# Kernel tuning notes

Measured on AMD Instinct MI355X. Metric: run time of the kernel, lower is better.

## Reference

```python
import jax, jax.numpy as jnp
import numpy as np

B, N, D_MODEL, H, LIN_K = 4, 4096, 1024, 16, 256
D_K = D_MODEL // H


def setup_inputs() -> dict:
    key = jax.random.key(0)
    ks = jax.random.split(key, 9)
    s = 1.0 / np.sqrt(D_MODEL)
    return {
        "K": jax.random.normal(ks[0], (B, N, D_MODEL), jnp.float32),
        "Q": jax.random.normal(ks[1], (B, N, D_MODEL), jnp.float32),
        "V": jax.random.normal(ks[2], (B, N, D_MODEL), jnp.float32),
        "We": jax.random.normal(ks[3], (N, LIN_K), jnp.float32) / np.sqrt(N),
        "be": jnp.zeros((LIN_K,), jnp.float32),
        "Wf": jax.random.normal(ks[4], (N, LIN_K), jnp.float32) / np.sqrt(N),
        "bf": jnp.zeros((LIN_K,), jnp.float32),
        "Wo": jax.random.normal(ks[5], (D_MODEL, D_MODEL), jnp.float32) * s,
        "bo": jnp.zeros((D_MODEL,), jnp.float32),
        "n_heads": H,
    }


def reference(K, Q, V, We, be, Wf, bf, Wo, bo, n_heads):
    b, n, d_model = K.shape
    d_k = d_model // n_heads
    split = lambda x: x.reshape(b, n, n_heads, d_k).transpose(0, 2, 1, 3)  # [b,h,n,d]
    Kh, Qh, Vh = split(K), split(Q), split(V)
    # Linformer projection: Dense(k) applied to K^T [b,h,d,n] -> [b,h,d,k]
    Kp = jnp.einsum("bhnd,nk->bhdk", Kh, We) + be
    scores = jnp.einsum("bhnd,bhdk->bhnk", Qh, Kp) / jnp.sqrt(jnp.float32(d_k))
    P = jax.nn.softmax(scores, axis=-1)  # dropout rate 0.0 -> identity
    # V projection: Dense(k) on V^T then transpose back -> [b,h,k,d]
    Vp = jnp.einsum("bhnd,nk->bhkd", Vh, Wf) + bf[:, None]
    out = jnp.einsum("bhnk,bhkd->bhnd", P, Vp)
    out = out.transpose(0, 2, 1, 3).reshape(b, n, d_model)
    return out @ Wo + bo
```

## Files before the change

### kernel.cpp

```cpp
#include <hip/hip_runtime.h>
#include <hip/hip_bf16.h>

#define BB      4
#define SEQ     4096
#define DMODEL  1024
#define NHEAD   16
#define DK      64
#define LK      256
#define BH      (BB*NHEAD)
#define SPLITK  4

typedef unsigned short u16;
typedef unsigned int   u32;
typedef float f32x4  __attribute__((ext_vector_type(4)));
typedef _Float16 f16x8 __attribute__((ext_vector_type(8)));

__device__ __forceinline__ u16 f2h(float f) {
    _Float16 h = (_Float16)f;
    u16 r; __builtin_memcpy(&r, &h, 2); return r;
}
__device__ __forceinline__ u32 packh(float a, float b) {
    return (u32)f2h(a) | ((u32)f2h(b) << 16);
}
__device__ __forceinline__ f16x8 pack8h(float4 a, float4 b) {
    union { uint4 u; f16x8 h; } r;
    r.u = make_uint4(packh(a.x, a.y), packh(a.z, a.w),
                     packh(b.x, b.y), packh(b.z, b.w));
    return r.h;
}
__device__ __forceinline__ void gl2lds16(const void* g, void* l) {
    __builtin_amdgcn_global_load_lds(
        (const __attribute__((address_space(1))) unsigned int*)g,
        (__attribute__((address_space(3))) unsigned int*)l,
        16, 0, 0);
}

__device__ __forceinline__ void tconv_body(
    const float* __restrict__ S, u16* __restrict__ D,
    int ss, int ds, int r0, int c0, int t)
{
    __shared__ float T[64][65];
    {
        int rr = (t >> 4) * 4;
        int cc = (t & 15) * 4;
#pragma unroll
        for (int i = 0; i < 4; ++i) {
            float4 v = *(const float4*)(S + (size_t)(r0 + rr + i) * ss + c0 + cc);
            T[rr + i][cc + 0] = v.x; T[rr + i][cc + 1] = v.y;
            T[rr + i][cc + 2] = v.z; T[rr + i][cc + 3] = v.w;
        }
    }
    __syncthreads();
    int cr = t >> 2, rc = (t & 3) * 16;
    u32 o[8];
#pragma unroll
    for (int j = 0; j < 8; ++j)
        o[j] = packh(T[rc + 2 * j][cr], T[rc + 2 * j + 1][cr]);
    u16* d = D + (size_t)(c0 + cr) * ds + r0 + rc;
    *(uint4*)(d)     = make_uint4(o[0], o[1], o[2], o[3]);
    *(uint4*)(d + 8) = make_uint4(o[4], o[5], o[6], o[7]);
}

__global__ __launch_bounds__(256) void tconv(
    const float* __restrict__ src, u16* __restrict__ dst,
    int ss, int ds, size_t sbo, size_t dbo)
{
    tconv_body(src + (size_t)blockIdx.z * sbo, dst + (size_t)blockIdx.z * dbo,
               ss, ds, blockIdx.x * 64, blockIdx.y * 64, threadIdx.x);
}

__global__ __launch_bounds__(256) void wo_convert(
    const float* __restrict__ Wo, u16* __restrict__ WoT)
{
    tconv_body(Wo, WoT, DMODEL, DMODEL, blockIdx.y * 64, blockIdx.x * 64, threadIdx.x);
}

__global__ __launch_bounds__(256) void tconv_all(
    const float* __restrict__ We, const float* __restrict__ Wf,
    const float* __restrict__ K,  const float* __restrict__ V,
    const float* __restrict__ Wo,
    u16* __restrict__ WeT, u16* __restrict__ WfT,
    u16* __restrict__ KT,  u16* __restrict__ VT, u16* __restrict__ WoT)
{
    const int id = blockIdx.x;
    const float* S; u16* D; int ss, ds, r0, c0;
    if (id < 512) {
        int j = id & 255;
        S  = (id < 256) ? We : Wf;
        D  = (id < 256) ? WeT : WfT;
        ss = LK; ds = SEQ;
        r0 = (j & 63) * 64; c0 = (j >> 6) * 64;
    } else if (id < 8704) {
        int j  = id - 512;
        int isV = j >= 4096; if (isV) j -= 4096;
        int bz = j >> 10, rem = j & 1023;
        S  = (isV ? V : K) + (size_t)bz * SEQ * DMODEL;
        D  = (isV ? VT : KT) + (size_t)bz * DMODEL * SEQ;
        ss = DMODEL; ds = SEQ;
        r0 = (rem & 63) * 64; c0 = (rem >> 6) * 64;
    } else {
        int j = id - 8704;
        S = Wo; D = WoT; ss = DMODEL; ds = DMODEL;
        r0 = (j & 15) * 64; c0 = (j >> 4) * 64;
    }
    tconv_body(S, D, ss, ds, r0, c0, threadIdx.x);
}

#define PROJ_BODY(Ab, Bb, bias, Cb, bias_on_row, c_row_stride, c0, r0)          \
    const int t  = threadIdx.x;                                                 \
    const int lane = t & 63;                                                    \
    const int w  = t >> 6;                                                      \
    const int wr = w >> 1, wc = w & 1;                                          \
    const int q  = lane >> 4, c = lane & 15;                                    \
    __shared__ u16 As[2][128 * 64];                                             \
    __shared__ u16 Bs[2][128 * 64];                                             \
    auto stage = [&](int buf, int kk) {                                         \
        _Pragma("unroll")                                                       \
        for (int i = 0; i < 4; ++i) {                                           \
            int li  = i * 256 + t;                                              \
            int row = li >> 3;                                                  \
            int c8  = (li & 7) ^ (row & 7);                                     \
            gl2lds16(Ab + (size_t)(r0 + row) * SEQ + kk + c8 * 8, &As[buf][(size_t)li * 8]); \
            gl2lds16(Bb + (size_t)(c0 + row) * SEQ + kk + c8 * 8, &Bs[buf][(size_t)li * 8]); \
        }                                                                       \
    };                                                                          \
    f32x4 acc[4][4];                                                            \
    _Pragma("unroll")                                                           \
    for (int m = 0; m < 4; ++m)                                                 \
        _Pragma("unroll")                                                       \
        for (int n = 0; n < 4; ++n) acc[m][n] = (f32x4){0.f, 0.f, 0.f, 0.f};    \
    stage(0, 0);                                                                \
    __syncthreads();                                                            \
    int cur = 0;                                                                \
    for (int k0 = 0; k0 < SEQ; k0 += 64) {                                      \
        if (k0 + 64 < SEQ) stage(cur ^ 1, k0 + 64);                             \
        _Pragma("unroll")                                                       \
        for (int s = 0; s < 2; ++s) {                                           \
            f16x8 af[4], bf[4];                                                 \
            _Pragma("unroll")                                                   \
            for (int m = 0; m < 4; ++m) {                                       \
                int row = wr * 64 + m * 16 + c;                                 \
                int c8  = (s * 4 + q) ^ (row & 7);                              \
                af[m] = *(const f16x8*)&As[cur][row * 64 + c8 * 8];             \
            }                                                                   \
            _Pragma("unroll")                                                   \
            for (int n = 0; n < 4; ++n) {                                       \
                int row = wc * 64 + n * 16 + c;                                 \
                int c8  = (s * 4 + q) ^ (row & 7);                              \
                bf[n] = *(const f16x8*)&Bs[cur][row * 64 + c8 * 8];             \
            }                                                                   \
            _Pragma("unroll")                                                   \
            for (int m = 0; m < 4; ++m)                                         \
                _Pragma("unroll")                                               \
                for (int n = 0; n < 4; ++n)                                     \
                    acc[m][n] = __builtin_amdgcn_mfma_f32_16x16x32_f16(af[m], bf[n], acc[m][n], 0, 0, 0); \
        }                                                                       \
        __syncthreads();                                                        \
        cur ^= 1;                                                               \
    }                                                                           \
    if (bias_on_row) {                                                          \
        _Pragma("unroll")                                                       \
        for (int m = 0; m < 4; ++m) {                                           \
            int rowb = r0 + wr * 64 + m * 16 + q * 4;                           \
            _Pragma("unroll")                                                   \
            for (int r = 0; r < 4; ++r) {                                       \
                float bv = bias[rowb + r];                                      \
                u16* dst = Cb + (size_t)(rowb + r) * c_row_stride + c0 + wc * 64 + c; \
                _Pragma("unroll")                                               \
                for (int n = 0; n < 4; ++n) dst[n * 16] = f2h(acc[m][n][r] + bv); \
            }                                                                   \
        }                                                                       \
    } else {                                                                    \
        float bv[4];                                                            \
        _Pragma("unroll")                                                       \
        for (int n = 0; n < 4; ++n) bv[n] = bias[c0 + wc * 64 + n * 16 + c];    \
        _Pragma("unroll")                                                       \
        for (int m = 0; m < 4; ++m) {                                           \
            int rowb = r0 + wr * 64 + m * 16 + q * 4;                           \
            _Pragma("unroll")                                                   \
            for (int r = 0; r < 4; ++r) {                                       \
                u16* dst = Cb + (size_t)(rowb + r) * c_row_stride + c0 + wc * 64 + c; \
                _Pragma("unroll")                                               \
                for (int n = 0; n < 4; ++n) dst[n * 16] = f2h(acc[m][n][r] + bv[n]); \
            }                                                                   \
        }                                                                       \
    }

__global__ __launch_bounds__(256) void proj_gemm(
    const u16* __restrict__ A, const u16* __restrict__ B,
    const float* __restrict__ bias, u16* __restrict__ Cout,
    int bias_on_row, size_t a_batch, size_t b_batch,
    int c_row_stride, size_t c_batch)
{
    const u16* Ab = A + (size_t)blockIdx.z * a_batch;
    const u16* Bb = B + (size_t)blockIdx.z * b_batch;
    u16* Cb       = Cout + (size_t)blockIdx.z * c_batch;
    const int c0 = blockIdx.x * 128;
    const int r0 = blockIdx.y * 128;
    PROJ_BODY(Ab, Bb, bias, Cb, bias_on_row, c_row_stride, c0, r0)
}

__global__ __launch_bounds__(256) void proj_both(
    const u16* __restrict__ WeT, const u16* __restrict__ WfT,
    const u16* __restrict__ KT,  const u16* __restrict__ VT,
    const float* __restrict__ be, const float* __restrict__ bfp,
    u16* __restrict__ KpF, u16* __restrict__ VpF)
{
    const int id = blockIdx.x;
    const u16 *Ab, *Bb; const float* bias; u16* Cb;
    int bias_on_row, c_row_stride, c0, r0;
    if (id < 64) {
        int b = id >> 4, s = id & 15;
        c0 = (s & 7) * 128; r0 = (s >> 3) * 128;
        Ab = WeT; Bb = KT + (size_t)b * DMODEL * SEQ;
        bias = be; bias_on_row = 1;
        Cb = KpF + (size_t)b * LK * DMODEL; c_row_stride = DMODEL;
    } else {
        int j = id - 64, b = j >> 4, s = j & 15;
        c0 = (s & 1) * 128; r0 = (s >> 1) * 128;
        Ab = VT + (size_t)b * DMODEL * SEQ; Bb = WfT;
        bias = bfp; bias_on_row = 0;
        Cb = VpF + (size_t)b * DMODEL * LK; c_row_stride = LK;
    }
    PROJ_BODY(Ab, Bb, bias, Cb, bias_on_row, c_row_stride, c0, r0)
}

__global__ __launch_bounds__(256) void proj_split(
    const u16* __restrict__ WeT, const u16* __restrict__ WfT,
    const u16* __restrict__ KT,  const u16* __restrict__ VT,
    float* __restrict__ PPK, float* __restrict__ PPV)
{
    const int sk = blockIdx.x >> 7;
    const int id = blockIdx.x & 127;
    const u16 *Ab, *Bb; float* Pout;
    int crs, c0, r0;
    if (id < 64) {
        int b = id >> 4, s = id & 15;
        c0 = (s & 7) * 128; r0 = (s >> 3) * 128;
        Ab = WeT; Bb = KT + (size_t)b * DMODEL * SEQ;
        Pout = PPK + ((size_t)sk * BB + b) * (LK * DMODEL); crs = DMODEL;
    } else {
        int j = id - 64, b = j >> 4, s = j & 15;
        c0 = (s & 1) * 128; r0 = (s >> 1) * 128;
        Ab = VT + (size_t)b * DMODEL * SEQ; Bb = WfT;
        Pout = PPV + ((size_t)sk * BB + b) * (DMODEL * LK); crs = LK;
    }
    const int kbeg = sk * (SEQ / SPLITK), kend = kbeg + SEQ / SPLITK;

    const int t  = threadIdx.x;
    const int lane = t & 63;
    const int w  = t >> 6;
    const int wr = w >> 1, wc = w & 1;
    const int q  = lane >> 4, c = lane & 15;
    __shared__ u16 As[2][128 * 64];
    __shared__ u16 Bs[2][128 * 64];
    auto stage = [&](int buf, int kk) {
#pragma unroll
        for (int i = 0; i < 4; ++i) {
            int li  = i * 256 + t;
            int row = li >> 3;
            int c8  = (li & 7) ^ (row & 7);
            gl2lds16(Ab + (size_t)(r0 + row) * SEQ + kk + c8 * 8, &As[buf][(size_t)li * 8]);
            gl2lds16(Bb + (size_t)(c0 + row) * SEQ + kk + c8 * 8, &Bs[buf][(size_t)li * 8]);
        }
    };
    f32x4 acc[4][4];
#pragma unroll
    for (int m = 0; m < 4; ++m)
#pragma unroll
        for (int n = 0; n < 4; ++n) acc[m][n] = (f32x4){0.f, 0.f, 0.f, 0.f};
    stage(0, kbeg);
    __syncthreads();
    int cur = 0;
    for (int k0 = kbeg; k0 < kend; k0 += 64) {
        if (k0 + 64 < kend) stage(cur ^ 1, k0 + 64);
#pragma unroll
        for (int s = 0; s < 2; ++s) {
            f16x8 af[4], bf[4];
#pragma unroll
            for (int m = 0; m < 4; ++m) {
                int row = wr * 64 + m * 16 + c;
                int c8  = (s * 4 + q) ^ (row & 7);
                af[m] = *(const f16x8*)&As[cur][row * 64 + c8 * 8];
            }
#pragma unroll
            for (int n = 0; n < 4; ++n) {
                int row = wc * 64 + n * 16 + c;
                int c8  = (s * 4 + q) ^ (row & 7);
                bf[n] = *(const f16x8*)&Bs[cur][row * 64 + c8 * 8];
            }
#pragma unroll
            for (int m = 0; m < 4; ++m)
#pragma unroll
                for (int n = 0; n < 4; ++n)
                    acc[m][n] = __builtin_amdgcn_mfma_f32_16x16x32_f16(af[m], bf[n], acc[m][n], 0, 0, 0);
        }
        __syncthreads();
        cur ^= 1;
    }
#pragma unroll
    for (int m = 0; m < 4; ++m) {
        int rowb = r0 + wr * 64 + m * 16 + q * 4;
#pragma unroll
        for (int r = 0; r < 4; ++r) {
            float* dst = Pout + (size_t)(rowb + r) * crs + c0 + wc * 64 + c;
#pragma unroll
            for (int n = 0; n < 4; ++n) dst[n * 16] = acc[m][n][r];
        }
    }
}

__global__ __launch_bounds__(256) void proj_reduce(
    const float* __restrict__ PPK, const float* __restrict__ PPV,
    const float* __restrict__ be,  const float* __restrict__ bfp,
    u16* __restrict__ KpF, u16* __restrict__ VpF)
{
    const int isV = blockIdx.y;
    const float* P    = isV ? PPV : PPK;
    const float* bias = isV ? bfp : be;
    u16* Out          = isV ? VpF : KpF;
    const size_t flat = ((size_t)blockIdx.x * 256 + threadIdx.x) * 4;
    const size_t skstride = (size_t)BB * LK * DMODEL;
    float4 a = *(const float4*)(P + flat);
#pragma unroll
    for (int sk = 1; sk < SPLITK; ++sk) {
        float4 p = *(const float4*)(P + (size_t)sk * skstride + flat);
        a.x += p.x; a.y += p.y; a.z += p.z; a.w += p.w;
    }
    if (!isV) {
        float bv = bias[(flat >> 10) & 255];
        a.x += bv; a.y += bv; a.z += bv; a.w += bv;
    } else {
        float4 bv = *(const float4*)(bias + (flat & 255));
        a.x += bv.x; a.y += bv.y; a.z += bv.z; a.w += bv.w;
    }
    uint2 o = make_uint2(packh(a.x, a.y), packh(a.z, a.w));
    *(uint2*)(Out + flat) = o;
}

__global__ __launch_bounds__(512) void attn_mfma(
    const float* __restrict__ Qin, const u16* __restrict__ KpF,
    const u16* __restrict__ VpF,   u16* __restrict__ AO)
{
    const int lin = blockIdx.x + blockIdx.y * gridDim.x;
    const int tid = (lin & 7) * 32 + (lin >> 3);
    const int bh = tid >> 2, b = bh >> 4, h = bh & 15;
    const int n0 = (tid & 3) * 1024;
    const int t  = threadIdx.x;
    const int w    = t >> 6;
    const int lane = t & 63;
    const int q    = lane >> 4;
    const int c    = lane & 15;

    __shared__ u16 Kl[16384];
    __shared__ u16 Vl[16384];
    __shared__ u16 Pl[128 * 264];

    const u16* kbase = KpF + (size_t)b * LK * DMODEL + h * DK;
#pragma unroll
    for (int i = 0; i < 4; ++i) {
        int li = i * 512 + t;
        int row = li >> 3, ch = li & 7;
        int chs = ch ^ (row & 7);
        gl2lds16(kbase + (size_t)row * DMODEL + chs * 8, Kl + (size_t)li * 8);
    }
    const u16* vbase = VpF + ((size_t)b * DMODEL + h * DK) * LK;
#pragma unroll
    for (int i = 0; i < 4; ++i) {
        int li = i * 512 + t;
        int row = li >> 5, ch = li & 31;
        int chs = (ch & 24) | ((ch & 7) ^ (row & 7));
        gl2lds16(vbase + (size_t)row * LK + chs * 8, Vl + (size_t)li * 8);
    }
    __syncthreads();

    const float* qbase = Qin + ((size_t)b * SEQ + n0 + w * 16 + c) * DMODEL + h * DK;
    const float4* qp0 = (const float4*)qbase;
    float4 q0 = qp0[2 * q], q1 = qp0[2 * q + 1];
    float4 q2 = qp0[8 + 2 * q], q3 = qp0[8 + 2 * q + 1];

    for (int p = 0; p < 8; ++p) {
        f16x8 a0 = pack8h(q0, q1);
        f16x8 a1 = pack8h(q2, q3);
        if (p < 7) {
            const float4* qp = (const float4*)(qbase + (size_t)(p + 1) * 128 * DMODEL);
            q0 = qp[2 * q]; q1 = qp[2 * q + 1];
            q2 = qp[8 + 2 * q]; q3 = qp[8 + 2 * q + 1];
        }

        f32x4 sc[16];
#pragma unroll
        for (int nt = 0; nt < 16; ++nt) sc[nt] = (f32x4){0.f, 0.f, 0.f, 0.f};
#pragma unroll
        for (int nt = 0; nt < 16; ++nt) {
            int ra = (nt * 16 + c) * 64;
            f16x8 b0 = *(const f16x8*)&Kl[ra + ((q ^ (c & 7)) * 8)];
            f16x8 b1 = *(const f16x8*)&Kl[ra + (((4 + q) ^ (c & 7)) * 8)];
            sc[nt] = __builtin_amdgcn_mfma_f32_16x16x32_f16(a0, b0, sc[nt], 0, 0, 0);
            sc[nt] = __builtin_amdgcn_mfma_f32_16x16x32_f16(a1, b1, sc[nt], 0, 0, 0);
        }

        float mx[4] = {-1e30f, -1e30f, -1e30f, -1e30f};
#pragma unroll
        for (int nt = 0; nt < 16; ++nt) {
            sc[nt] *= 0.125f;
#pragma unroll
            for (int r = 0; r < 4; ++r) mx[r] = fmaxf(mx[r], sc[nt][r]);
        }
#pragma unroll
        for (int d = 1; d < 16; d <<= 1)
#pragma unroll
            for (int r = 0; r < 4; ++r) mx[r] = fmaxf(mx[r], __shfl_xor(mx[r], d, 64));

        float sm[4] = {0.f, 0.f, 0.f, 0.f};
#pragma unroll
        for (int nt = 0; nt < 16; ++nt)
#pragma unroll
            for (int r = 0; r < 4; ++r) {
                float e = __expf(sc[nt][r] - mx[r]);
                sc[nt][r] = e;
                sm[r] += e;
            }
#pragma unroll
        for (int d = 1; d < 16; d <<= 1)
#pragma unroll
            for (int r = 0; r < 4; ++r) sm[r] += __shfl_xor(sm[r], d, 64);
        float inv[4];
#pragma unroll
        for (int r = 0; r < 4; ++r) inv[r] = 1.0f / sm[r];

#pragma unroll
        for (int nt = 0; nt < 16; ++nt)
#pragma unroll
            for (int r = 0; r < 4; ++r)
                Pl[(w * 16 + q * 4 + r) * 264 + nt * 16 + c] = f2h(sc[nt][r] * inv[r]);

        f32x4 ov[4];
#pragma unroll
        for (int nt = 0; nt < 4; ++nt) ov[nt] = (f32x4){0.f, 0.f, 0.f, 0.f};
#pragma unroll
        for (int ks = 0; ks < 8; ++ks) {
            f16x8 pa = *(const f16x8*)&Pl[(w * 16 + c) * 264 + ks * 32 + q * 8];
#pragma unroll
            for (int nt = 0; nt < 4; ++nt) {
                int chunk = ks * 4 + q;
                int chs = (chunk & 24) | ((chunk & 7) ^ (c & 7));
                f16x8 vf = *(const f16x8*)&Vl[(nt * 16 + c) * 256 + chs * 8];
                ov[nt] = __builtin_amdgcn_mfma_f32_16x16x32_f16(pa, vf, ov[nt], 0, 0, 0);
            }
        }

#pragma unroll
        for (int nt = 0; nt < 4; ++nt)
#pragma unroll
            for (int r = 0; r < 4; ++r)
                Pl[(w * 16 + q * 4 + r) * 264 + nt * 16 + c] = f2h(ov[nt][r]);

#pragma unroll
        for (int ps = 0; ps < 2; ++ps) {
            int lr  = w * 16 + ps * 8 + (lane >> 3);
            int col = (lane & 7) * 8;
            uint4 vv = *(uint4*)&Pl[lr * 264 + col];
            *(uint4*)(AO + ((size_t)b * SEQ + n0 + p * 128 + lr) * DMODEL + h * DK + col) = vv;
        }
    }
}

#define OBM 128
#define OBN 128
#define OBK 64

__global__ __launch_bounds__(256) void out_gemm_mfma(
    const u16* __restrict__ AO, const u16* __restrict__ WoT,
    const float* __restrict__ bo, float* __restrict__ Out)
{
    const int lin = blockIdx.x + blockIdx.y * gridDim.x;
    const int tid = (lin & 7) * 128 + (lin >> 3);
    const int r0 = (tid >> 3) * OBM;
    const int c0 = (tid & 7) * OBN;
    const int t  = threadIdx.x;
    const int lane = t & 63;
    const int w  = t >> 6;
    const int wr = w >> 1, wc = w & 1;
    const int q  = lane >> 4, c = lane & 15;

    __shared__ u16 As[OBM * OBK];
    __shared__ u16 Bs[OBN * OBK];

    f32x4 acc[4][4];
#pragma unroll
    for (int m = 0; m < 4; ++m)
#pragma unroll
        for (int n = 0; n < 4; ++n) acc[m][n] = (f32x4){0.f, 0.f, 0.f, 0.f};

    for (int k0 = 0; k0 < DMODEL; k0 += OBK) {
#pragma unroll
        for (int i = 0; i < 4; ++i) {
            int li  = i * 256 + t;
            int row = li >> 3;
            int c8  = (li & 7) ^ (row & 7);
            gl2lds16(AO  + (size_t)(r0 + row) * DMODEL + k0 + c8 * 8, (u16*)As + (size_t)li * 8);
            gl2lds16(WoT + (size_t)(c0 + row) * DMODEL + k0 + c8 * 8, (u16*)Bs + (size_t)li * 8);
        }
        __syncthreads();

#pragma unroll
        for (int s = 0; s < 2; ++s) {
            f16x8 af[4], bf[4];
#pragma unroll
            for (int m = 0; m < 4; ++m) {
                int row = wr * 64 + m * 16 + c;
                int c8  = (s * 4 + q) ^ (row & 7);
                af[m] = *(const f16x8*)&As[row * 64 + c8 * 8];
            }
#pragma unroll
            for (int n = 0; n < 4; ++n) {
                int row = wc * 64 + n * 16 + c;
                int c8  = (s * 4 + q) ^ (row & 7);
                bf[n] = *(const f16x8*)&Bs[row * 64 + c8 * 8];
            }
#pragma unroll
            for (int m = 0; m < 4; ++m)
#pragma unroll
                for (int n = 0; n < 4; ++n)
                    acc[m][n] = __builtin_amdgcn_mfma_f32_16x16x32_f16(af[m], bf[n], acc[m][n], 0, 0, 0);
        }
        __syncthreads();
    }

    float bv[4];
#pragma unroll
    for (int n = 0; n < 4; ++n) bv[n] = bo[c0 + wc * 64 + n * 16 + c];
#pragma unroll
    for (int m = 0; m < 4; ++m) {
        int rowb = r0 + wr * 64 + m * 16 + q * 4;
#pragma unroll
        for (int r = 0; r < 4; ++r) {
            float* dst = Out + (size_t)(rowb + r) * DMODEL + c0 + wc * 64 + c;
#pragma unroll
            for (int n = 0; n < 4; ++n) dst[n * 16] = acc[m][n][r] + bv[n];
        }
    }
}

extern "C" void kernel_launch(void* const* d_in, const int* in_sizes, int n_in,
                              void* d_out, int out_size, void* d_ws, size_t ws_size,
                              hipStream_t stream)
{
    const float* K   = (const float*)d_in[0];
    const float* Q   = (const float*)d_in[1];
    const float* V   = (const float*)d_in[2];
    const float* We  = (const float*)d_in[3];
    const float* be  = (const float*)d_in[4];
    const float* Wf  = (const float*)d_in[5];
    const float* bfp = (const float*)d_in[6];
    const float* Wo  = (const float*)d_in[7];
    const float* bo  = (const float*)d_in[8];
    float* Out = (float*)d_out;

    const size_t M1 = 1048576;
    const size_t TB = (size_t)BB * DMODEL * SEQ;
    const size_t PFLOATS = (size_t)SPLITK * BB * LK * DMODEL;
    const size_t NEED_SPLIT = (5 * M1 + 2 * TB) * 2 + 2 * PFLOATS * 4;
    const size_t NEED_PAR   = 2 * (4 * M1 + 2 * TB);

    if (ws_size >= NEED_SPLIT) {
        u16* KpF = (u16*)d_ws;
        u16* VpF = KpF + M1;
        u16* WeT = VpF + M1;
        u16* WfT = WeT + M1;
        u16* WoT = WfT + M1;
        u16* KT  = WoT + M1;
        u16* VT  = KT + TB;
        float* PPK = (float*)(VT + TB);
        float* PPV = PPK + PFLOATS;
        u16* AO  = KT;

        tconv_all<<<dim3(8960), 256, 0, stream>>>(We, Wf, K, V, Wo, WeT, WfT, KT, VT, WoT);
        proj_split<<<dim3(128 * SPLITK), 256, 0, stream>>>(WeT, WfT, KT, VT, PPK, PPV);
        proj_reduce<<<dim3(1024, 2), 256, 0, stream>>>(PPK, PPV, be, bfp, KpF, VpF);
        attn_mfma<<<dim3(4, BH), 512, 0, stream>>>(Q, KpF, VpF, AO);
        out_gemm_mfma<<<dim3(DMODEL / OBN, (BB * SEQ) / OBM), 256, 0, stream>>>(AO, WoT, bo, Out);
    } else if (ws_size >= NEED_PAR) {
        u16* KpF = (u16*)d_ws;
        u16* VpF = KpF + M1;
        u16* WeT = VpF + M1;
        u16* WfT = WeT + M1;
        u16* KT  = WfT + M1;
        u16* VT  = KT + TB;
        u16* AO  = KT;
        u16* WoT = WeT;

        tconv<<<dim3(SEQ / 64, LK / 64, 1), 256, 0, stream>>>(We, WeT, LK, SEQ, 0, 0);
        tconv<<<dim3(SEQ / 64, LK / 64, 1), 256, 0, stream>>>(Wf, WfT, LK, SEQ, 0, 0);
        tconv<<<dim3(SEQ / 64, DMODEL / 64, BB), 256, 0, stream>>>(
            K, KT, DMODEL, SEQ, (size_t)SEQ * DMODEL, (size_t)DMODEL * SEQ);
        tconv<<<dim3(SEQ / 64, DMODEL / 64, BB), 256, 0, stream>>>(
            V, VT, DMODEL, SEQ, (size_t)SEQ * DMODEL, (size_t)DMODEL * SEQ);
        proj_both<<<dim3(128), 256, 0, stream>>>(WeT, WfT, KT, VT, be, bfp, KpF, VpF);
        wo_convert<<<dim3(DMODEL / 64, DMODEL / 64), 256, 0, stream>>>(Wo, WoT);
        attn_mfma<<<dim3(4, BH), 512, 0, stream>>>(Q, KpF, VpF, AO);
        out_gemm_mfma<<<dim3(DMODEL / OBN, (BB * SEQ) / OBM), 256, 0, stream>>>(AO, WoT, bo, Out);
    } else {
        u16* KpF = (u16*)d_ws;
        u16* VpF = KpF + (size_t)BB * LK * DMODEL;
        u16* BIG = VpF + (size_t)BB * DMODEL * LK;
        u16* Wsm = BIG + (size_t)BB * SEQ * DMODEL;

        tconv<<<dim3(SEQ / 64, LK / 64, 1), 256, 0, stream>>>(We, Wsm, LK, SEQ, 0, 0);
        tconv<<<dim3(SEQ / 64, DMODEL / 64, BB), 256, 0, stream>>>(
            K, BIG, DMODEL, SEQ, (size_t)SEQ * DMODEL, (size_t)DMODEL * SEQ);
        proj_gemm<<<dim3(DMODEL / 128, LK / 128, BB), 256, 0, stream>>>(
            Wsm, BIG, be, KpF, 1, (size_t)0, (size_t)DMODEL * SEQ, DMODEL, (size_t)LK * DMODEL);
        tconv<<<dim3(SEQ / 64, LK / 64, 1), 256, 0, stream>>>(Wf, Wsm, LK, SEQ, 0, 0);
        tconv<<<dim3(SEQ / 64, DMODEL / 64, BB), 256, 0, stream>>>(
            V, BIG, DMODEL, SEQ, (size_t)SEQ * DMODEL, (size_t)DMODEL * SEQ);
        proj_gemm<<<dim3(LK / 128, DMODEL / 128, BB), 256, 0, stream>>>(
            BIG, Wsm, bfp, VpF, 0, (size_t)DMODEL * SEQ, (size_t)0, LK, (size_t)DMODEL * LK);
        wo_convert<<<dim3(DMODEL / 64, DMODEL / 64), 256, 0, stream>>>(Wo, Wsm);
        attn_mfma<<<dim3(4, BH), 512, 0, stream>>>(Q, KpF, VpF, BIG);
        out_gemm_mfma<<<dim3(DMODEL / OBN, (BB * SEQ) / OBM), 256, 0, stream>>>(BIG, Wsm, bo, Out);
    }
}
```

Measured before the change: 337.5 us.

## Use 128-row transpose tiles and stage output GEMM stores through LDS

```diff
diff --git a/kernel.cpp b/kernel.cpp
--- a/kernel.cpp
+++ b/kernel.cpp
@@ -75,6 +75,34 @@
     tconv_body(Wo, WoT, DMODEL, DMODEL, blockIdx.y * 64, blockIdx.x * 64, threadIdx.x);
 }
 
+__device__ __forceinline__ void tconv_body128(
+    const float* __restrict__ S, u16* __restrict__ D,
+    int ss, int ds, int r0, int c0, int t)
+{
+    __shared__ float T[128][72];
+    {
+        int rr = t >> 4;
+        int cc = (t & 15) * 4;
+#pragma unroll
+        for (int i = 0; i < 8; ++i) {
+            float4 v = *(const float4*)(S + (size_t)(r0 + rr + i * 16) * ss + c0 + cc);
+            float* dst = &T[rr + i * 16][cc];
+            dst[0] = v.x; dst[1] = v.y; dst[2] = v.z; dst[3] = v.w;
+        }
+    }
+    __syncthreads();
+    int cr = t >> 2, rc = (t & 3) * 32;
+    u32 o[16];
+#pragma unroll
+    for (int j = 0; j < 16; ++j)
+        o[j] = packh(T[rc + 2 * j][cr], T[rc + 2 * j + 1][cr]);
+    u16* d = D + (size_t)(c0 + cr) * ds + r0 + rc;
+    *(uint4*)(d)      = make_uint4(o[0],  o[1],  o[2],  o[3]);
+    *(uint4*)(d + 8)  = make_uint4(o[4],  o[5],  o[6],  o[7]);
+    *(uint4*)(d + 16) = make_uint4(o[8],  o[9],  o[10], o[11]);
+    *(uint4*)(d + 24) = make_uint4(o[12], o[13], o[14], o[15]);
+}
+
 __global__ __launch_bounds__(256) void tconv_all(
     const float* __restrict__ We, const float* __restrict__ Wf,
     const float* __restrict__ K,  const float* __restrict__ V,
@@ -84,26 +112,26 @@
 {
     const int id = blockIdx.x;
     const float* S; u16* D; int ss, ds, r0, c0;
-    if (id < 512) {
-        int j = id & 255;
-        S  = (id < 256) ? We : Wf;
-        D  = (id < 256) ? WeT : WfT;
+    if (id < 256) {
+        int j = id & 127;
+        S  = (id < 128) ? We : Wf;
+        D  = (id < 128) ? WeT : WfT;
         ss = LK; ds = SEQ;
-        r0 = (j & 63) * 64; c0 = (j >> 6) * 64;
-    } else if (id < 8704) {
-        int j  = id - 512;
-        int isV = j >= 4096; if (isV) j -= 4096;
-        int bz = j >> 10, rem = j & 1023;
+        r0 = (j & 31) * 128; c0 = (j >> 5) * 64;
+    } else if (id < 4352) {
+        int j  = id - 256;
+        int isV = j >= 2048; if (isV) j -= 2048;
+        int bz = j >> 9, rem = j & 511;
         S  = (isV ? V : K) + (size_t)bz * SEQ * DMODEL;
         D  = (isV ? VT : KT) + (size_t)bz * DMODEL * SEQ;
         ss = DMODEL; ds = SEQ;
-        r0 = (rem & 63) * 64; c0 = (rem >> 6) * 64;
+        r0 = (rem & 31) * 128; c0 = (rem >> 5) * 64;
     } else {
-        int j = id - 8704;
+        int j = id - 4352;
         S = Wo; D = WoT; ss = DMODEL; ds = DMODEL;
-        r0 = (j & 15) * 64; c0 = (j >> 4) * 64;
-    }
-    tconv_body(S, D, ss, ds, r0, c0, threadIdx.x);
+        r0 = (j & 7) * 128; c0 = (j >> 3) * 64;
+    }
+    tconv_body128(S, D, ss, ds, r0, c0, threadIdx.x);
 }
 
 #define PROJ_BODY(Ab, Bb, bias, Cb, bias_on_row, c_row_stride, c0, r0)          \
@@ -486,6 +514,7 @@
 
     __shared__ u16 As[OBM * OBK];
     __shared__ u16 Bs[OBN * OBK];
+    __shared__ float Ol[4][16][68];
 
     f32x4 acc[4][4];
 #pragma unroll
@@ -533,12 +562,18 @@
     for (int n = 0; n < 4; ++n) bv[n] = bo[c0 + wc * 64 + n * 16 + c];
 #pragma unroll
     for (int m = 0; m < 4; ++m) {
-        int rowb = r0 + wr * 64 + m * 16 + q * 4;
-#pragma unroll
-        for (int r = 0; r < 4; ++r) {
-            float* dst = Out + (size_t)(rowb + r) * DMODEL + c0 + wc * 64 + c;
-#pragma unroll
-            for (int n = 0; n < 4; ++n) dst[n * 16] = acc[m][n][r] + bv[n];
+#pragma unroll
+        for (int r = 0; r < 4; ++r)
+#pragma unroll
+            for (int n = 0; n < 4; ++n)
+                Ol[w][q * 4 + r][n * 16 + c] = acc[m][n][r] + bv[n];
+#pragma unroll
+        for (int i = 0; i < 4; ++i) {
+            int rl = (lane >> 4) + i * 4;
+            float4 v = *(const float4*)&Ol[w][rl][(lane & 15) * 4];
+            float* dst = Out + (size_t)(r0 + wr * 64 + m * 16 + rl) * DMODEL
+                       + c0 + wc * 64 + (lane & 15) * 4;
+            *(float4*)dst = v;
         }
     }
 }
@@ -576,7 +611,7 @@
         float* PPV = PPK + PFLOATS;
         u16* AO  = KT;
 
-        tconv_all<<<dim3(8960), 256, 0, stream>>>(We, Wf, K, V, Wo, WeT, WfT, KT, VT, WoT);
+        tconv_all<<<dim3(4480), 256, 0, stream>>>(We, Wf, K, V, Wo, WeT, WfT, KT, VT, WoT);
         proj_split<<<dim3(128 * SPLITK), 256, 0, stream>>>(WeT, WfT, KT, VT, PPK, PPV);
         proj_reduce<<<dim3(1024, 2), 256, 0, stream>>>(PPK, PPV, be, bfp, KpF, VpF);
         attn_mfma<<<dim3(4, BH), 512, 0, stream>>>(Q, KpF, VpF, AO);
```

New measurement: 338.8 us. Within noise of the previous version (+0.4%).
